# Performance work log

Measured on AMD Instinct MI355X. Metric: run time of the kernel, lower is better.

## Reference

```python
import jax, jax.numpy as jnp
import numpy as np

N_NODES = 500_000
N_FEAT = 125          # embedding dim; cat with pos(3) -> 128
HIDDEN = 128
OUT_DIM = 64
N_TYPES = 100
N_GRAPHS = 4096


def setup_inputs() -> dict:
    key = jax.random.key(0)
    ks = jax.random.split(key, 10)
    pos = jax.random.normal(ks[0], (N_NODES, 3), dtype=jnp.float32)
    z = jax.random.randint(ks[1], (N_NODES,), 0, N_TYPES)
    batch = jnp.sort(jax.random.randint(ks[2], (N_NODES,), 0, N_GRAPHS))
    emb = jax.random.normal(ks[3], (N_TYPES, N_FEAT), dtype=jnp.float32)
    s1 = 1.0 / np.sqrt(N_FEAT + 3)
    s2 = 1.0 / np.sqrt(HIDDEN)
    W1 = jax.random.normal(ks[4], (N_FEAT + 3, HIDDEN), dtype=jnp.float32) * s1
    b1 = jnp.zeros((HIDDEN,), dtype=jnp.float32)
    W2 = jax.random.normal(ks[5], (HIDDEN, HIDDEN), dtype=jnp.float32) * s2
    b2 = jnp.zeros((HIDDEN,), dtype=jnp.float32)
    W3 = jax.random.normal(ks[6], (HIDDEN, OUT_DIM), dtype=jnp.float32) * s2
    b3 = jnp.zeros((OUT_DIM,), dtype=jnp.float32)
    return {"pos": pos, "z": z, "batch": batch, "emb": emb,
            "W1": W1, "b1": b1, "W2": W2, "b2": b2, "W3": W3, "b3": b3}


def reference(pos, z, batch, emb, W1, b1, W2, b2, W3, b3):
    # embed node types and concat with 3D positions  -> [N, 128]
    x = jnp.concatenate([pos, emb[z]], axis=-1)
    # two equivariant-transformer layers (per-node transform) + relu
    x = jax.nn.relu(x @ W1 + b1)   # [N, H]
    x = jax.nn.relu(x @ W2 + b2)   # [N, H]
    # output head
    x = x @ W3 + b3                # [N, O]
    # global mean pool per graph
    s = jax.ops.segment_sum(x, batch, num_segments=N_GRAPHS)                    # [G, O]
    cnt = jax.ops.segment_sum(jnp.ones((x.shape[0], 1), x.dtype), batch,
                              num_segments=N_GRAPHS)                            # [G, 1]
    return s / jnp.maximum(cnt, 1.0)
```

## Files before the change

kernel.cpp:

```cpp
#include <hip/hip_runtime.h>
#include <hip/hip_bf16.h>

#define N_NODES 500000
#define N_FEAT 125
#define HID 128
#define OUTD 64
#define N_GRAPHS 4096
#define N_TYPES 100
#define NPAIRS 7813
#define NBLOCKS 256
#define NWAVES 8
#define TPAD 132

typedef float f32x4 __attribute__((ext_vector_type(4)));
typedef short s16x4 __attribute__((ext_vector_type(4)));

#define OFF_T 0
#define SZ_T (N_TYPES * TPAD * 4)
#define OFF_W2K (OFF_T + SZ_T)
#define SZ_W2K (8 * 8 * 64 * 8)
#define OFF_W3K (OFF_W2K + SZ_W2K)
#define SZ_W3K (4 * 8 * 64 * 8)
#define OFF_B2 (OFF_W3K + SZ_W3K)
#define LDS_BYTES (OFF_B2 + HID * 4)

#define WS_GSUM 0
#define WS_GCNT ((size_t)N_GRAPHS * OUTD * 4)
#define WS_T    (WS_GCNT + (size_t)N_GRAPHS * 4)
#define WS_ZERO WS_T
#define WS_ZERO_V4 (WS_ZERO / 16)

__device__ __forceinline__ unsigned short f2bf(float f) {
  union { float f; unsigned u; } v; v.f = f;
  unsigned r = v.u + 0x7FFFu + ((v.u >> 16) & 1u);
  return (unsigned short)(r >> 16);
}
__device__ __forceinline__ unsigned pk2bf(float a, float b) {
  __hip_bfloat162 h = __float22bfloat162_rn(float2{a, b});
  union { __hip_bfloat162 h; unsigned u; } v; v.h = h;
  return v.u;
}
__device__ __forceinline__ s16x4 u2frag(uint2 v) {
  union { uint2 u; s16x4 s; } c; c.u = v; return c.s;
}

extern "C" __global__ void gnn_prep(const float* __restrict__ emb,
                                    const float* __restrict__ W1,
                                    const float* __restrict__ b1,
                                    float* __restrict__ Tgf,
                                    f32x4* __restrict__ wsz)
{
  const int j = threadIdx.x;
  const int tid = blockIdx.x * 128 + j;
  for (int i = tid; i < WS_ZERO_V4; i += 256 * 128)
    wsz[i] = (f32x4){0.f, 0.f, 0.f, 0.f};
  const int g = blockIdx.x;
  if (g < N_TYPES) {
    float acc = b1[j];
    const float* er = emb + g * N_FEAT;
    for (int k = 0; k < N_FEAT; ++k)
      acc = fmaf(er[k], W1[(3 + k) * HID + j], acc);
    Tgf[g * HID + j] = acc;
  }
}

extern "C" __global__ void __launch_bounds__(512, 2)
gnn_main(const float* __restrict__ pos, const int* __restrict__ z,
         const int* __restrict__ batch, const float* __restrict__ Tgf,
         const float* __restrict__ W1, const float* __restrict__ W2,
         const float* __restrict__ b2, const float* __restrict__ W3,
         float* __restrict__ gsum, int* __restrict__ gcnt)
{
  extern __shared__ char lds[];
  float* Tl = (float*)(lds + OFF_T);
  uint2* w2k = (uint2*)(lds + OFF_W2K);
  uint2* w3k = (uint2*)(lds + OFF_W3K);
  float* bias2 = (float*)(lds + OFF_B2);

  const int t = threadIdx.x;

  for (int i = t; i < N_TYPES * HID; i += 512) {
    int g = i >> 7, f = i & 127;
    Tl[g * TPAD + f] = Tgf[i];
  }
  for (int i = t; i < 8 * 8 * 64; i += 512) {
    int oi = i >> 9, ki = (i >> 6) & 7, ln = i & 63;
    int q = ln >> 4, l = ln & 15;
    int f0 = ki * 16 + q * 4, o = oi * 16 + l;
    uint2 v;
    v.x = pk2bf(W2[(f0 + 0) * HID + o], W2[(f0 + 1) * HID + o]);
    v.y = pk2bf(W2[(f0 + 2) * HID + o], W2[(f0 + 3) * HID + o]);
    w2k[i] = v;
  }
  for (int i = t; i < 4 * 8 * 64; i += 512) {
    int ob = i >> 9, rest = i & 511;
    int oi = rest >> 6, ln = rest & 63;
    int q = ln >> 4, l = ln & 15;
    int f0 = oi * 16 + q * 4, o = ob * 16 + l;
    uint2 v;
    v.x = pk2bf(W3[(f0 + 0) * OUTD + o], W3[(f0 + 1) * OUTD + o]);
    v.y = pk2bf(W3[(f0 + 2) * OUTD + o], W3[(f0 + 3) * OUTD + o]);
    w3k[i] = v;
  }
  if (t < HID) bias2[t] = b2[t];

  const int wave = t >> 6, lane = t & 63, quad = lane >> 4, l15 = lane & 15;

  uint2 wa1[8];
  #pragma unroll
  for (int oi = 0; oi < 8; ++oi) {
    if (quad == 0) {
      const int f = oi * 16 + l15;
      unsigned lo = (unsigned)f2bf(W1[f]) | ((unsigned)f2bf(W1[HID + f]) << 16);
      unsigned hi = (unsigned)f2bf(W1[2 * HID + f]);
      wa1[oi] = uint2{lo, hi};
    } else {
      wa1[oi] = uint2{0u, 0u};
    }
  }

  __syncthreads();

  const int gwave = blockIdx.x * NWAVES + wave;

  for (int pair = gwave; pair < NPAIRS; pair += NBLOCKS * NWAVES) {
    const int base = pair * 64;
    const bool has2 = (pair != NPAIRS - 1);

    int id0 = batch[base + l15];
    int id1 = batch[base + 16 + l15];
    int id2 = -1, id3 = -1;
    if (has2) {
      id2 = batch[base + 32 + l15];
      id3 = batch[base + 48 + l15];
    }

    int Toff[4];
    uint2 bpos[4];
    #pragma unroll
    for (int m = 0; m < 4; ++m) {
      int node = base + m * 16 + l15;
      node = node < N_NODES ? node : N_NODES - 1;
      Toff[m] = z[node] * TPAD + quad * 4;
      const float px = pos[node * 3], py = pos[node * 3 + 1], pz = pos[node * 3 + 2];
      bpos[m] = (quad == 0) ? uint2{pk2bf(px, py), pk2bf(pz, 0.f)} : uint2{0u, 0u};
    }

    uint2 a16[8][4];
    __builtin_amdgcn_s_setprio(1);
    #pragma unroll
    for (int oi = 0; oi < 8; ++oi)
      #pragma unroll
      for (int m = 0; m < 4; ++m) {
        f32x4 cc = *(const f32x4*)(Tl + Toff[m] + oi * 16);
        cc = __builtin_amdgcn_mfma_f32_16x16x16bf16_1k(
            u2frag(wa1[oi]), u2frag(bpos[m]), cc, 0, 0, 0);
        a16[oi][m].x = pk2bf(fmaxf(cc[0], 0.f), fmaxf(cc[1], 0.f));
        a16[oi][m].y = pk2bf(fmaxf(cc[2], 0.f), fmaxf(cc[3], 0.f));
      }
    __builtin_amdgcn_s_setprio(0);

    uint2 pb[8][4];
    __builtin_amdgcn_s_setprio(1);
    #pragma unroll
    for (int oi = 0; oi < 8; ++oi) {
      f32x4 bv = *(const f32x4*)(bias2 + oi * 16 + quad * 4);
      f32x4 c[4] = {bv, bv, bv, bv};
      #pragma unroll
      for (int ki = 0; ki < 8; ++ki) {
        s16x4 wa = u2frag(w2k[(oi * 8 + ki) * 64 + lane]);
        #pragma unroll
        for (int m = 0; m < 4; ++m)
          c[m] = __builtin_amdgcn_mfma_f32_16x16x16bf16_1k(
              wa, u2frag(a16[ki][m]), c[m], 0, 0, 0);
      }
      #pragma unroll
      for (int m = 0; m < 4; ++m) {
        pb[oi][m].x = pk2bf(fmaxf(c[m][0], 0.f), fmaxf(c[m][1], 0.f));
        pb[oi][m].y = pk2bf(fmaxf(c[m][2], 0.f), fmaxf(c[m][3], 0.f));
      }
    }
    __builtin_amdgcn_s_setprio(0);

    f32x4 acc3[4][4] = {};
    __builtin_amdgcn_s_setprio(1);
    #pragma unroll
    for (int ob = 0; ob < 4; ++ob)
      #pragma unroll
      for (int oi = 0; oi < 8; ++oi) {
        s16x4 wa = u2frag(w3k[(ob * 8 + oi) * 64 + lane]);
        #pragma unroll
        for (int m = 0; m < 4; ++m)
          acc3[ob][m] = __builtin_amdgcn_mfma_f32_16x16x16bf16_1k(
              wa, u2frag(pb[oi][m]), acc3[ob][m], 0, 0, 0);
      }
    __builtin_amdgcn_s_setprio(0);

    {
      const int NT = has2 ? 64 : 32;
      int done = 0;
      while (done < NT) {
        const int sel = done >> 4;
        int srcv = (sel & 2) ? ((sel & 1) ? id3 : id2)
                             : ((sel & 1) ? id1 : id0);
        const int g = __builtin_amdgcn_readlane(srcv, done & 15);
        const bool m0 = (id0 == g), m1 = (id1 == g), m2 = (id2 == g), m3 = (id3 == g);
        float red[4][4];
        #pragma unroll
        for (int ob = 0; ob < 4; ++ob)
          #pragma unroll
          for (int r = 0; r < 4; ++r)
            red[ob][r] = (m0 ? acc3[ob][0][r] : 0.f) + (m1 ? acc3[ob][1][r] : 0.f)
                       + (m2 ? acc3[ob][2][r] : 0.f) + (m3 ? acc3[ob][3][r] : 0.f);
        #pragma unroll
        for (int s = 1; s <= 8; s <<= 1)
          #pragma unroll
          for (int ob = 0; ob < 4; ++ob)
            #pragma unroll
            for (int r = 0; r < 4; ++r)
              red[ob][r] += __shfl_xor(red[ob][r], s, 64);
        const int cnt = (int)((__popcll(__ballot(m0)) + __popcll(__ballot(m1)) +
                               __popcll(__ballot(m2)) + __popcll(__ballot(m3))) >> 2);
        if (l15 == 0) {
          #pragma unroll
          for (int ob = 0; ob < 4; ++ob)
            #pragma unroll
            for (int r = 0; r < 4; ++r)
              atomicAdd(&gsum[g * OUTD + ob * 16 + quad * 4 + r], red[ob][r]);
        }
        if (lane == 0) atomicAdd(&gcnt[g], cnt);
        done += cnt;
      }
    }
  }
}

extern "C" __global__ void gnn_finalize(const float* __restrict__ gsum,
                                        const int* __restrict__ gcnt,
                                        const float* __restrict__ b3,
                                        float* __restrict__ out)
{
  int i = blockIdx.x * 256 + threadIdx.x;
  if (i < N_GRAPHS * OUTD) {
    int g = i >> 6, o = i & 63;
    int c = gcnt[g];
    out[i] = (c > 0) ? (gsum[i] / (float)c + b3[o]) : 0.f;
  }
}

extern "C" void kernel_launch(void* const* d_in, const int* in_sizes, int n_in,
                              void* d_out, int out_size, void* d_ws, size_t ws_size,
                              hipStream_t stream) {
  const float* pos  = (const float*)d_in[0];
  const int*   z    = (const int*)d_in[1];
  const int*   batch= (const int*)d_in[2];
  const float* emb  = (const float*)d_in[3];
  const float* W1   = (const float*)d_in[4];
  const float* b1   = (const float*)d_in[5];
  const float* W2   = (const float*)d_in[6];
  const float* b2   = (const float*)d_in[7];
  const float* W3   = (const float*)d_in[8];
  const float* b3   = (const float*)d_in[9];

  float* gsum = (float*)d_ws;
  int*   gcnt = (int*)((char*)d_ws + WS_GCNT);
  float* Tgf  = (float*)((char*)d_ws + WS_T);

  hipLaunchKernelGGL(gnn_prep, dim3(256), dim3(HID), 0, stream,
                     emb, W1, b1, Tgf, (f32x4*)d_ws);

  hipFuncSetAttribute((const void*)gnn_main,
                      hipFuncAttributeMaxDynamicSharedMemorySize, LDS_BYTES);
  hipLaunchKernelGGL(gnn_main, dim3(NBLOCKS), dim3(512), LDS_BYTES, stream,
                     pos, z, batch, Tgf, W1, W2, b2, W3, gsum, gcnt);
  hipLaunchKernelGGL(gnn_finalize, dim3((N_GRAPHS * OUTD + 255) / 256), dim3(256), 0, stream,
                     gsum, gcnt, b3, (float*)d_out);
}
```

Before: 138.1 us.

## Use 16x16x32 bf16 MFMA for layer 2 with bpermute fragment repacking

Layer 2 now uses the wider 16x16x32 bf16 MFMA, halving the number of matrix instructions per output tile. W2 is stored in LDS as a transposed, padded bf16 matrix so each lane reads an 8-element fragment with one vector load. Layer-1 outputs are regrouped into the 8-element K layout using ds_bpermute cross-lane shuffles. This adds LDS permute traffic and select instructions in exchange for fewer MFMA issues and fewer W2 loads.

New measurement: 135.9 us. Within noise of the previous version (-1.7%).

```diff
diff --git a/kernel.cpp b/kernel.cpp
--- a/kernel.cpp
+++ b/kernel.cpp
@@ -11,15 +11,17 @@
 #define NBLOCKS 256
 #define NWAVES 8
 #define TPAD 132
+#define WPAD 136
 
 typedef float f32x4 __attribute__((ext_vector_type(4)));
+typedef short s16x8 __attribute__((ext_vector_type(8)));
 typedef short s16x4 __attribute__((ext_vector_type(4)));
 
 #define OFF_T 0
 #define SZ_T (N_TYPES * TPAD * 4)
-#define OFF_W2K (OFF_T + SZ_T)
-#define SZ_W2K (8 * 8 * 64 * 8)
-#define OFF_W3K (OFF_W2K + SZ_W2K)
+#define OFF_W2 (OFF_T + SZ_T)
+#define SZ_W2 (HID * WPAD * 2)
+#define OFF_W3K (OFF_W2 + SZ_W2)
 #define SZ_W3K (4 * 8 * 64 * 8)
 #define OFF_B2 (OFF_W3K + SZ_W3K)
 #define LDS_BYTES (OFF_B2 + HID * 4)
@@ -73,7 +75,7 @@
 {
   extern __shared__ char lds[];
   float* Tl = (float*)(lds + OFF_T);
-  uint2* w2k = (uint2*)(lds + OFF_W2K);
+  unsigned short* w2t = (unsigned short*)(lds + OFF_W2);
   uint2* w3k = (uint2*)(lds + OFF_W3K);
   float* bias2 = (float*)(lds + OFF_B2);
 
@@ -83,14 +85,9 @@
     int g = i >> 7, f = i & 127;
     Tl[g * TPAD + f] = Tgf[i];
   }
-  for (int i = t; i < 8 * 8 * 64; i += 512) {
-    int oi = i >> 9, ki = (i >> 6) & 7, ln = i & 63;
-    int q = ln >> 4, l = ln & 15;
-    int f0 = ki * 16 + q * 4, o = oi * 16 + l;
-    uint2 v;
-    v.x = pk2bf(W2[(f0 + 0) * HID + o], W2[(f0 + 1) * HID + o]);
-    v.y = pk2bf(W2[(f0 + 2) * HID + o], W2[(f0 + 3) * HID + o]);
-    w2k[i] = v;
+  for (int i = t; i < HID * HID; i += 512) {
+    int k = i >> 7, n = i & 127;
+    w2t[n * WPAD + k] = f2bf(W2[i]);
   }
   for (int i = t; i < 4 * 8 * 64; i += 512) {
     int ob = i >> 9, rest = i & 511;
@@ -105,6 +102,9 @@
   if (t < HID) bias2[t] = b2[t];
 
   const int wave = t >> 6, lane = t & 63, quad = lane >> 4, l15 = lane & 15;
+  const bool hi32 = (lane >= 32);
+  const int A0 = ((((lane >> 4) & 1) << 5) + l15) << 2;
+  const int A1 = A0 + 64;
 
   uint2 wa1[8];
   #pragma unroll
@@ -146,18 +146,36 @@
       bpos[m] = (quad == 0) ? uint2{pk2bf(px, py), pk2bf(pz, 0.f)} : uint2{0u, 0u};
     }
 
-    uint2 a16[8][4];
+    s16x8 an[4][4];
     __builtin_amdgcn_s_setprio(1);
     #pragma unroll
-    for (int oi = 0; oi < 8; ++oi)
+    for (int kb = 0; kb < 4; ++kb) {
+      uint2 Ps[2][4];
+      #pragma unroll
+      for (int s = 0; s < 2; ++s) {
+        const int oi = 2 * kb + s;
+        #pragma unroll
+        for (int m = 0; m < 4; ++m) {
+          f32x4 cc = *(const f32x4*)(Tl + Toff[m] + oi * 16);
+          cc = __builtin_amdgcn_mfma_f32_16x16x16bf16_1k(
+              u2frag(wa1[oi]), u2frag(bpos[m]), cc, 0, 0, 0);
+          Ps[s][m].x = pk2bf(fmaxf(cc[0], 0.f), fmaxf(cc[1], 0.f));
+          Ps[s][m].y = pk2bf(fmaxf(cc[2], 0.f), fmaxf(cc[3], 0.f));
+        }
+      }
       #pragma unroll
       for (int m = 0; m < 4; ++m) {
-        f32x4 cc = *(const f32x4*)(Tl + Toff[m] + oi * 16);
-        cc = __builtin_amdgcn_mfma_f32_16x16x16bf16_1k(
-            u2frag(wa1[oi]), u2frag(bpos[m]), cc, 0, 0, 0);
-        a16[oi][m].x = pk2bf(fmaxf(cc[0], 0.f), fmaxf(cc[1], 0.f));
-        a16[oi][m].y = pk2bf(fmaxf(cc[2], 0.f), fmaxf(cc[3], 0.f));
-      }
+        s16x8 fr;
+        #pragma unroll
+        for (int j2 = 0; j2 < 4; ++j2) {
+          const int addr = (j2 < 2) ? A0 : A1;
+          int t0 = __builtin_amdgcn_ds_bpermute(addr, (int)((j2 & 1) ? Ps[0][m].y : Ps[0][m].x));
+          int t1 = __builtin_amdgcn_ds_bpermute(addr, (int)((j2 & 1) ? Ps[1][m].y : Ps[1][m].x));
+          ((int*)&fr)[j2] = hi32 ? t1 : t0;
+        }
+        an[m][kb] = fr;
+      }
+    }
     __builtin_amdgcn_s_setprio(0);
 
     uint2 pb[8][4];
@@ -167,12 +185,11 @@
       f32x4 bv = *(const f32x4*)(bias2 + oi * 16 + quad * 4);
       f32x4 c[4] = {bv, bv, bv, bv};
       #pragma unroll
-      for (int ki = 0; ki < 8; ++ki) {
-        s16x4 wa = u2frag(w2k[(oi * 8 + ki) * 64 + lane]);
+      for (int k = 0; k < 4; ++k) {
+        s16x8 w = *(const s16x8*)(w2t + (oi * 16 + l15) * WPAD + k * 32 + quad * 8);
         #pragma unroll
         for (int m = 0; m < 4; ++m)
-          c[m] = __builtin_amdgcn_mfma_f32_16x16x16bf16_1k(
-              wa, u2frag(a16[ki][m]), c[m], 0, 0, 0);
+          c[m] = __builtin_amdgcn_mfma_f32_16x16x32_bf16(w, an[m][k], c[m], 0, 0, 0);
       }
       #pragma unroll
       for (int m = 0; m < 4; ++m) {
```
